# Kernel optimization log

Measured on AMD Instinct MI355X. Metric: run time of the kernel, lower is better.

Reference implementation:

```python
import jax, jax.numpy as jnp
import numpy as np

K = 3            # mc_sampling_steps
ALPHA = 0.5      # importance-weight decay
LAMBDA_COV = 0.5
EPS = 1e-8


def setup_inputs() -> dict:
    key = jax.random.key(0)
    k1, k2, k3, k4 = jax.random.split(key, 4)
    B, S, Et, Es, Ht, Hs = 8, 4096, 128, 16, 2048, 1024
    tg = jax.random.uniform(k1, (B, S, Et)) + 1e-3
    tg = tg / tg.sum(-1, keepdims=True)          # teacher gate probs
    sg = jax.random.uniform(k2, (B, S, Es)) + 1e-3
    sg = sg / sg.sum(-1, keepdims=True)          # student gate probs
    th = jax.random.normal(k3, (B, S, Ht))
    sh = jax.random.normal(k4, (B, S, Hs))
    am = jnp.ones((B, S), dtype=jnp.int32)       # all tokens valid
    return {"teacher_gates": tg, "student_gates": sg,
            "teacher_hidden_states": th, "student_hidden_states": sh,
            "attention_mask": am}


def _method_a(teacher_gates, student_gates, attention_mask):
    B, S, Et = teacher_gates.shape
    Es = student_gates.shape[-1]
    N = B * S
    tp = teacher_gates.reshape(N, Et)                 # flat teacher probs [N, Et]
    sp = student_gates.reshape(N, Es)                 # flat student probs [N, Es]
    log_sp = jnp.log(sp)
    vm = attention_mask.reshape(N).astype(tp.dtype)   # valid-token mask [N]
    carry_f = Et // Es                                # expert_dist[::carry] stride
    rows = jnp.arange(N)

    def step(carry, _):
        probs, key = carry
        key, sub = jax.random.split(key)
        idx = jax.random.categorical(sub, jnp.log(probs), axis=-1)        # multinomial [N]
        w = jnp.take_along_axis(probs, idx[:, None], axis=1)[:, 0]        # importance wt
        new = probs.at[rows, idx].multiply(ALPHA)                         # damp sampled expert
        new = new / new.sum(-1, keepdims=True)
        return (new, key), (idx, w)

    (_, _), (idxs, ws) = jax.lax.scan(step, (tp, jax.random.key(42)), None, length=K)
    ws = ws * vm[None, :]                             # [K, N]

    # KL(one_hot(idx)[::carry] || student) = -log sp[i, idx//carry] iff idx % carry == 0
    sidx = jnp.clip(idxs // carry_f, 0, Es - 1)
    hit = (idxs % carry_f) == 0
    kl = jnp.where(hit, -log_sp[rows[None, :], sidx], 0.0)                # [K, N]
    total_weight = ws.sum()
    feat_loss = (kl * ws).sum() / jnp.maximum(total_weight, EPS)

    # expert coverage counts (only teacher experts with index < Es contribute)
    in_range = (idxs < Es).astype(tp.dtype)
    t_counts = jnp.zeros(Et, tp.dtype).at[idxs.reshape(-1)].add((ws * in_range).reshape(-1))
    sval = sp[rows[None, :], jnp.clip(idxs, 0, Es - 1)] * in_range * vm[None, :]
    s_counts = jnp.zeros(Et, tp.dtype).at[idxs.reshape(-1)].add(sval.reshape(-1))

    ta = t_counts / t_counts.sum()
    sa = s_counts / s_counts.sum()
    ta = (ta + EPS); ta = ta / ta.sum()
    sa = (sa + EPS); sa = sa / sa.sum()
    coverage_kl = jnp.sum(ta * (jnp.log(ta) - jnp.log(sa))) / Et          # batchmean over Et
    return feat_loss, coverage_kl, feat_loss + LAMBDA_COV * coverage_kl


def reference(teacher_gates, student_gates, teacher_hidden_states, student_hidden_states, attention_mask):
    # enable_method_a=True, enable_method_b=False -> expert_total_loss == method_a_total_loss
    _, _, total = _method_a(teacher_gates, student_gates, attention_mask)
    return total
```

## Files before the change

### kernel.cpp

```cpp
#include <hip/hip_runtime.h>
#include <stdint.h>

#define ET 128
#define ES 16
#define ACC_STRIDE 258
#define ACC_USED 34
#define MAX_REPL 64

__host__ __device__ inline uint32_t rotl32(uint32_t x, int r) {
#ifdef __HIP_DEVICE_COMPILE__
  return __builtin_amdgcn_alignbit(x, x, (uint32_t)(32 - r));
#else
  return (x << r) | (x >> (32 - r));
#endif
}

__host__ __device__ inline void tf2x32(uint32_t k0, uint32_t k1,
                                       uint32_t& x0, uint32_t& x1) {
  uint32_t ks2 = k0 ^ k1 ^ 0x1BD11BDAu;
  x0 += k0; x1 += k1;
#define TF_ROT(r) { x0 += x1; x1 = rotl32(x1, r); x1 ^= x0; }
  TF_ROT(13) TF_ROT(15) TF_ROT(26) TF_ROT(6)
  x0 += k1;  x1 += ks2 + 1u;
  TF_ROT(17) TF_ROT(29) TF_ROT(16) TF_ROT(24)
  x0 += ks2; x1 += k0 + 2u;
  TF_ROT(13) TF_ROT(15) TF_ROT(26) TF_ROT(6)
  x0 += k0;  x1 += k1 + 3u;
  TF_ROT(17) TF_ROT(29) TF_ROT(16) TF_ROT(24)
  x0 += k1;  x1 += ks2 + 4u;
  TF_ROT(13) TF_ROT(15) TF_ROT(26) TF_ROT(6)
  x0 += ks2; x1 += k0 + 5u;
#undef TF_ROT
}

__device__ inline float unif01(uint32_t s0, uint32_t s1, uint32_t j) {
  uint32_t x0 = 0u, x1 = j;
  tf2x32(s0, s1, x0, x1);
  uint32_t bits = x0 ^ x1;
  float f = __uint_as_float((bits >> 9) | 0x3F800000u) - 1.0f;
  const float TINY = 1.17549435e-38f;
  return fmaxf(TINY, f + TINY);
}

__launch_bounds__(256)
__global__ void sample_kernel(const float* __restrict__ tg,
                              const float* __restrict__ sg,
                              const int* __restrict__ am,
                              double* __restrict__ acc,
                              unsigned int* __restrict__ done,
                              float* __restrict__ out,
                              int repl,
                              uint32_t s00, uint32_t s01,
                              uint32_t s10, uint32_t s11,
                              uint32_t s20, uint32_t s21,
                              int N, int total_waves) {
  __shared__ float lds_t[ES], lds_s[ES];
  __shared__ float lds_w[4], lds_kl[4];
  __shared__ int lds_last;
  __shared__ double tot[ACC_USED];
  if (threadIdx.x < ES) { lds_t[threadIdx.x] = 0.f; lds_s[threadIdx.x] = 0.f; }
  __syncthreads();

  const int wslot = threadIdx.x >> 6;
  const int wid = blockIdx.x * 4 + wslot;
  const int lane = threadIdx.x & 63;
  const int gl = lane & 15;
  const int gbase = lane & 0x30;
  const int stride = total_waves * 4;

  float sum_w = 0.f, sum_kl = 0.f;

#define LOADT(BASE, P, SGV, VM)                                              \
  {                                                                          \
    int nr_ = (BASE) + (lane >> 4);                                          \
    int ok_ = (nr_ < N);                                                     \
    int n_ = ok_ ? nr_ : (N - 1);                                            \
    const float4* r4_ = (const float4*)(tg + (size_t)n_ * ET + gl * 8);      \
    float4 aa_ = r4_[0], bb_ = r4_[1];                                       \
    P[0] = aa_.x; P[1] = aa_.y; P[2] = aa_.z; P[3] = aa_.w;                  \
    P[4] = bb_.x; P[5] = bb_.y; P[6] = bb_.z; P[7] = bb_.w;                  \
    SGV = sg[(size_t)n_ * ES + gl];                                          \
    VM = ok_ ? (float)am[n_] : 0.f;                                          \
  }

#define STEP(KA, KB, LAST)                                                   \
  {                                                                          \
    float e[8];                                                              \
    _Pragma("unroll")                                                        \
    for (int q = 0; q < 8; ++q)                                              \
      e[q] = -__logf(unif01(KA, KB, jb + (uint32_t)q)) * inv[q];             \
    unsigned long long key = ~0ull, ko;                                      \
    _Pragma("unroll")                                                        \
    for (int q = 0; q < 8; ++q) {                                            \
      ko = ((unsigned long long)__float_as_uint(e[q]) << 32)                 \
           | (uint32_t)(ebase + q);                                          \
      if (ko < key) key = ko;                                                \
    }                                                                        \
    ko = __shfl_xor(key, 1); if (ko < key) key = ko;                         \
    ko = __shfl_xor(key, 2); if (ko < key) key = ko;                         \
    ko = __shfl_xor(key, 4); if (ko < key) key = ko;                         \
    ko = __shfl_xor(key, 8); if (ko < key) key = ko;                         \
    const int bi = (int)(key & 0xFFu);                                       \
    const int wl = bi >> 3, wslt = bi & 7;                                   \
    float pw = p[0];                                                         \
    _Pragma("unroll")                                                        \
    for (int q = 1; q < 8; ++q) pw = (wslt == q) ? p[q] : pw;                \
    float w_abs = __shfl(pw, gbase | wl);                                    \
    float sgkl = __shfl(sgv, gbase | wl);                                    \
    float sgcv = __shfl(sgv, gbase | (bi & 15));                             \
    float wsv = w_abs * __frcp_rn(t) * vm;                                   \
    const bool lead = (gl == 0);                                             \
    sum_w += lead ? wsv : 0.f;                                               \
    float klt = ((bi & 7) == 0) ? (-__logf(sgkl)) * wsv : 0.f;               \
    sum_kl += lead ? klt : 0.f;                                              \
    if (lead && bi < ES) {                                                   \
      atomicAdd(&lds_t[bi], wsv);                                            \
      atomicAdd(&lds_s[bi], sgcv * vm);                                      \
    }                                                                        \
    if (!(LAST)) {                                                           \
      const bool mt = (gl == wl);                                            \
      _Pragma("unroll")                                                      \
      for (int q = 0; q < 8; ++q) {                                          \
        bool hit = mt && (wslt == q);                                        \
        p[q] = hit ? p[q] * 0.5f : p[q];                                     \
        inv[q] = hit ? inv[q] * 2.0f : inv[q];                               \
      }                                                                      \
      t -= 0.5f * w_abs;                                                     \
    }                                                                        \
  }

  float p[8], sgv = 0.f, vm = 0.f;
  const int base0 = wid * 4;
  if (base0 < N) LOADT(base0, p, sgv, vm);

  for (int base = base0; base < N; base += stride) {
    const int nxt = base + stride;
    float pn[8] = {0, 0, 0, 0, 0, 0, 0, 0};
    float sgn = 0.f, vmn = 0.f;
    if (nxt < N) LOADT(nxt, pn, sgn, vmn);

    {
      int nr = base + (lane >> 4);
      int n_ = (nr < N) ? nr : (N - 1);
      const uint32_t jb = (uint32_t)n_ * ET + (uint32_t)(gl * 8);
      const int ebase = gl * 8;
      float inv[8];
#pragma unroll
      for (int q = 0; q < 8; ++q) inv[q] = __frcp_rn(p[q]);
      float t = 1.0f;
      STEP(s00, s01, 0)
      STEP(s10, s11, 0)
      STEP(s20, s21, 1)
    }

#pragma unroll
    for (int q = 0; q < 8; ++q) p[q] = pn[q];
    sgv = sgn; vm = vmn;
  }
#undef STEP
#undef LOADT

#pragma unroll
  for (int off = 32; off; off >>= 1) {
    sum_w += __shfl_xor(sum_w, off);
    sum_kl += __shfl_xor(sum_kl, off);
  }
  if (lane == 0) { lds_w[wslot] = sum_w; lds_kl[wslot] = sum_kl; }
  __syncthreads();

  double* slot = acc + (size_t)(blockIdx.x % repl) * ACC_STRIDE;
  if (threadIdx.x == 0) {
    atomicAdd(&slot[0], (double)(lds_w[0] + lds_w[1] + lds_w[2] + lds_w[3]));
    atomicAdd(&slot[1], (double)(lds_kl[0] + lds_kl[1] + lds_kl[2] + lds_kl[3]));
  }
  if (threadIdx.x < ES) {
    atomicAdd(&slot[2 + threadIdx.x], (double)lds_t[threadIdx.x]);
    atomicAdd(&slot[2 + ES + threadIdx.x], (double)lds_s[threadIdx.x]);
  }

  if (threadIdx.x == 0) {
    __threadfence();
    unsigned prev = atomicAdd(done, 1u);
    lds_last = (prev == (unsigned)(gridDim.x - 1)) ? 1 : 0;
  }
  __syncthreads();
  if (!lds_last) return;

  const int tid = threadIdx.x;
  if (tid < ACC_USED) tot[tid] = 0.0;
  __syncthreads();
  for (int idx = tid; idx < repl * ACC_USED; idx += 256) {
    int r = idx / ACC_USED, f = idx - r * ACC_USED;
    double v = __hip_atomic_load(&acc[(size_t)r * ACC_STRIDE + f],
                                 __ATOMIC_RELAXED, __HIP_MEMORY_SCOPE_AGENT);
    atomicAdd(&tot[f], v);
  }
  __syncthreads();

  const double EPSD = 1e-8;
  double tv = (tid < ES) ? tot[2 + tid] : 0.0;
  double sv = (tid < ES) ? tot[2 + ES + tid] : 0.0;
  double tsum = tv, ssum = sv;
#pragma unroll
  for (int off = 8; off; off >>= 1) {
    tsum += __shfl_xor(tsum, off);
    ssum += __shfl_xor(ssum, off);
  }
  double ta = tv / tsum + EPSD;
  double sa = sv / ssum + EPSD;
  double ta2 = (tid < ES) ? ta : 0.0;
  double sa2 = (tid < ES) ? sa : 0.0;
#pragma unroll
  for (int off = 8; off; off >>= 1) {
    ta2 += __shfl_xor(ta2, off);
    sa2 += __shfl_xor(sa2, off);
  }
  ta2 += (double)(ET - ES) * EPSD;
  sa2 += (double)(ET - ES) * EPSD;
  double tn = ta / ta2, sn = sa / sa2;
  double ci = (tid < ES) ? tn * (log(tn) - log(sn)) : 0.0;
#pragma unroll
  for (int off = 8; off; off >>= 1) ci += __shfl_xor(ci, off);

  if (tid == 0) {
    double ta0 = EPSD / ta2, sa0 = EPSD / sa2;
    double cov = ci + (double)(ET - ES) * ta0 * (log(ta0) - log(sa0));
    cov /= (double)ET;
    double feat = tot[1] / fmax(tot[0], EPSD);
    out[0] = (float)(feat + 0.5 * cov);
  }
}

extern "C" void kernel_launch(void* const* d_in, const int* in_sizes, int n_in,
                              void* d_out, int out_size, void* d_ws, size_t ws_size,
                              hipStream_t stream) {
  const float* tg = (const float*)d_in[0];
  const float* sg = (const float*)d_in[1];
  const int*   am = (const int*)d_in[4];
  const int N = in_sizes[4];

  uint32_t key0 = 0u, key1 = 42u;
  uint32_t subs[3][2];
  for (int k = 0; k < 3; ++k) {
    uint32_t a0 = 0u, a1 = 0u; tf2x32(key0, key1, a0, a1);
    uint32_t b0 = 0u, b1 = 1u; tf2x32(key0, key1, b0, b1);
    subs[k][0] = b0; subs[k][1] = b1;
    key0 = a0; key1 = a1;
  }

  int repl = (int)((ws_size - 256) / (ACC_STRIDE * sizeof(double)));
  if (repl > MAX_REPL) repl = MAX_REPL;
  if (repl < 1) repl = 1;

  double* acc = (double*)d_ws;
  unsigned int* done = (unsigned int*)((char*)d_ws + (size_t)repl * ACC_STRIDE * sizeof(double));
  hipMemsetAsync(d_ws, 0, (size_t)repl * ACC_STRIDE * sizeof(double) + 64, stream);

  int blocks = (N + 31) / 32;
  if (blocks > 2048) blocks = 2048;
  if (blocks < 1) blocks = 1;
  const int total_waves = blocks * 4;

  sample_kernel<<<blocks, 256, 0, stream>>>(
      tg, sg, am, acc, done, (float*)d_out, repl,
      subs[0][0], subs[0][1], subs[1][0], subs[1][1], subs[2][0], subs[2][1],
      N, total_waves);
}
```

Measured before the change: 52.21 us.

## Use DPP min-reduction, 32-bit keys, log2 sampling, and drop software prefetch

Switches the per-row argmin to 32-bit packed keys reduced with DPP row operations instead of 64-bit shuffles. It replaces -log with log2 times a folded -ln2/p factor, uses the approximate rcp, and drops the TINY clamp on the uniform. It also removes the register double-buffered prefetch, fixes the replica count at 16, and shrinks the grid so each block covers fewer rows. The truncated key mantissa and the missing clamp can change tie-breaking and edge cases relative to the reference.

```diff
diff --git a/kernel.cpp b/kernel.cpp
--- a/kernel.cpp
+++ b/kernel.cpp
@@ -5,7 +5,7 @@
 #define ES 16
 #define ACC_STRIDE 258
 #define ACC_USED 34
-#define MAX_REPL 64
+#define REPL 16
 
 __host__ __device__ inline uint32_t rotl32(uint32_t x, int r) {
 #ifdef __HIP_DEVICE_COMPILE__
@@ -33,13 +33,19 @@
 #undef TF_ROT
 }
 
-__device__ inline float unif01(uint32_t s0, uint32_t s1, uint32_t j) {
+__device__ inline float unif01m(uint32_t s0, uint32_t s1, uint32_t j) {
   uint32_t x0 = 0u, x1 = j;
   tf2x32(s0, s1, x0, x1);
   uint32_t bits = x0 ^ x1;
-  float f = __uint_as_float((bits >> 9) | 0x3F800000u) - 1.0f;
-  const float TINY = 1.17549435e-38f;
-  return fmaxf(TINY, f + TINY);
+  return __uint_as_float((bits >> 9) | 0x3F800000u) - 1.0f;
+}
+
+__device__ inline float fastrcp(float x) { return __builtin_amdgcn_rcpf(x); }
+
+template <int CTRL>
+__device__ inline uint32_t dpp32(uint32_t v) {
+  return (uint32_t)__builtin_amdgcn_update_dpp((int)v, (int)v, CTRL, 0xF, 0xF,
+                                               false);
 }
 
 __launch_bounds__(256)
@@ -49,7 +55,6 @@
                               double* __restrict__ acc,
                               unsigned int* __restrict__ done,
                               float* __restrict__ out,
-                              int repl,
                               uint32_t s00, uint32_t s01,
                               uint32_t s10, uint32_t s11,
                               uint32_t s20, uint32_t s21,
@@ -67,40 +72,30 @@
   const int gl = lane & 15;
   const int gbase = lane & 0x30;
   const int stride = total_waves * 4;
+  const float NLN2 = -0.69314718055994530942f;
 
   float sum_w = 0.f, sum_kl = 0.f;
-
-#define LOADT(BASE, P, SGV, VM)                                              \
-  {                                                                          \
-    int nr_ = (BASE) + (lane >> 4);                                          \
-    int ok_ = (nr_ < N);                                                     \
-    int n_ = ok_ ? nr_ : (N - 1);                                            \
-    const float4* r4_ = (const float4*)(tg + (size_t)n_ * ET + gl * 8);      \
-    float4 aa_ = r4_[0], bb_ = r4_[1];                                       \
-    P[0] = aa_.x; P[1] = aa_.y; P[2] = aa_.z; P[3] = aa_.w;                  \
-    P[4] = bb_.x; P[5] = bb_.y; P[6] = bb_.z; P[7] = bb_.w;                  \
-    SGV = sg[(size_t)n_ * ES + gl];                                          \
-    VM = ok_ ? (float)am[n_] : 0.f;                                          \
-  }
 
 #define STEP(KA, KB, LAST)                                                   \
   {                                                                          \
     float e[8];                                                              \
     _Pragma("unroll")                                                        \
     for (int q = 0; q < 8; ++q)                                              \
-      e[q] = -__logf(unif01(KA, KB, jb + (uint32_t)q)) * inv[q];             \
-    unsigned long long key = ~0ull, ko;                                      \
+      e[q] = __log2f(unif01m(KA, KB, jb + (uint32_t)q)) * invn[q];           \
+    uint32_t key = 0xFFFFFFFFu;                                              \
     _Pragma("unroll")                                                        \
     for (int q = 0; q < 8; ++q) {                                            \
-      ko = ((unsigned long long)__float_as_uint(e[q]) << 32)                 \
-           | (uint32_t)(ebase + q);                                          \
-      if (ko < key) key = ko;                                                \
-    }                                                                        \
-    ko = __shfl_xor(key, 1); if (ko < key) key = ko;                         \
-    ko = __shfl_xor(key, 2); if (ko < key) key = ko;                         \
-    ko = __shfl_xor(key, 4); if (ko < key) key = ko;                         \
-    ko = __shfl_xor(key, 8); if (ko < key) key = ko;                         \
-    const int bi = (int)(key & 0xFFu);                                       \
+      uint32_t kq = (__float_as_uint(e[q]) & 0xFFFFFF80u)                    \
+                    | (uint32_t)(ebase + q);                                 \
+      key = (kq < key) ? kq : key;                                           \
+    }                                                                        \
+    { uint32_t o;                                                            \
+      o = dpp32<0x128>(key); key = (o < key) ? o : key;       \
+      o = dpp32<0x124>(key); key = (o < key) ? o : key;       \
+      o = dpp32<0x122>(key); key = (o < key) ? o : key;       \
+      o = dpp32<0x121>(key); key = (o < key) ? o : key;       \
+    }                                                                        \
+    const int bi = (int)(key & 0x7Fu);                                       \
     const int wl = bi >> 3, wslt = bi & 7;                                   \
     float pw = p[0];                                                         \
     _Pragma("unroll")                                                        \
@@ -108,10 +103,10 @@
     float w_abs = __shfl(pw, gbase | wl);                                    \
     float sgkl = __shfl(sgv, gbase | wl);                                    \
     float sgcv = __shfl(sgv, gbase | (bi & 15));                             \
-    float wsv = w_abs * __frcp_rn(t) * vm;                                   \
+    float wsv = w_abs * fastrcp(t) * vm;                                     \
     const bool lead = (gl == 0);                                             \
     sum_w += lead ? wsv : 0.f;                                               \
-    float klt = ((bi & 7) == 0) ? (-__logf(sgkl)) * wsv : 0.f;               \
+    float klt = (wslt == 0) ? (-__logf(sgkl)) * wsv : 0.f;                   \
     sum_kl += lead ? klt : 0.f;                                              \
     if (lead && bi < ES) {                                                   \
       atomicAdd(&lds_t[bi], wsv);                                            \
@@ -123,42 +118,35 @@
       for (int q = 0; q < 8; ++q) {                                          \
         bool hit = mt && (wslt == q);                                        \
         p[q] = hit ? p[q] * 0.5f : p[q];                                     \
-        inv[q] = hit ? inv[q] * 2.0f : inv[q];                               \
+        invn[q] = hit ? invn[q] * 2.0f : invn[q];                            \
       }                                                                      \
       t -= 0.5f * w_abs;                                                     \
     }                                                                        \
   }
 
-  float p[8], sgv = 0.f, vm = 0.f;
-  const int base0 = wid * 4;
-  if (base0 < N) LOADT(base0, p, sgv, vm);
-
-  for (int base = base0; base < N; base += stride) {
-    const int nxt = base + stride;
-    float pn[8] = {0, 0, 0, 0, 0, 0, 0, 0};
-    float sgn = 0.f, vmn = 0.f;
-    if (nxt < N) LOADT(nxt, pn, sgn, vmn);
-
-    {
-      int nr = base + (lane >> 4);
-      int n_ = (nr < N) ? nr : (N - 1);
-      const uint32_t jb = (uint32_t)n_ * ET + (uint32_t)(gl * 8);
-      const int ebase = gl * 8;
-      float inv[8];
-#pragma unroll
-      for (int q = 0; q < 8; ++q) inv[q] = __frcp_rn(p[q]);
-      float t = 1.0f;
-      STEP(s00, s01, 0)
-      STEP(s10, s11, 0)
-      STEP(s20, s21, 1)
-    }
-
-#pragma unroll
-    for (int q = 0; q < 8; ++q) p[q] = pn[q];
-    sgv = sgn; vm = vmn;
+  for (int base = wid * 4; base < N; base += stride) {
+    const int nr = base + (lane >> 4);
+    const int ok = (nr < N);
+    const int n = ok ? nr : (N - 1);
+
+    const float4* r4 = (const float4*)(tg + (size_t)n * ET + gl * 8);
+    float4 aa = r4[0], bb = r4[1];
+    float p[8] = {aa.x, aa.y, aa.z, aa.w, bb.x, bb.y, bb.z, bb.w};
+    float sgv = sg[(size_t)n * ES + gl];
+    float vm = ok ? (float)am[n] : 0.f;
+
+    float invn[8];
+#pragma unroll
+    for (int q = 0; q < 8; ++q) invn[q] = NLN2 * fastrcp(p[q]);
+
+    float t = 1.0f;
+    const uint32_t jb = (uint32_t)n * ET + (uint32_t)(gl * 8);
+    const int ebase = gl * 8;
+    STEP(s00, s01, 0)
+    STEP(s10, s11, 0)
+    STEP(s20, s21, 1)
   }
 #undef STEP
-#undef LOADT
 
 #pragma unroll
   for (int off = 32; off; off >>= 1) {
@@ -168,7 +156,7 @@
   if (lane == 0) { lds_w[wslot] = sum_w; lds_kl[wslot] = sum_kl; }
   __syncthreads();
 
-  double* slot = acc + (size_t)(blockIdx.x % repl) * ACC_STRIDE;
+  double* slot = acc + (size_t)(blockIdx.x % REPL) * ACC_STRIDE;
   if (threadIdx.x == 0) {
     atomicAdd(&slot[0], (double)(lds_w[0] + lds_w[1] + lds_w[2] + lds_w[3]));
     atomicAdd(&slot[1], (double)(lds_kl[0] + lds_kl[1] + lds_kl[2] + lds_kl[3]));
@@ -187,13 +175,12 @@
   if (!lds_last) return;
 
   const int tid = threadIdx.x;
-  if (tid < ACC_USED) tot[tid] = 0.0;
-  __syncthreads();
-  for (int idx = tid; idx < repl * ACC_USED; idx += 256) {
-    int r = idx / ACC_USED, f = idx - r * ACC_USED;
-    double v = __hip_atomic_load(&acc[(size_t)r * ACC_STRIDE + f],
-                                 __ATOMIC_RELAXED, __HIP_MEMORY_SCOPE_AGENT);
-    atomicAdd(&tot[f], v);
+  if (tid < ACC_USED) {
+    double s = 0.0;
+    for (int r = 0; r < REPL; ++r)
+      s += __hip_atomic_load(&acc[(size_t)r * ACC_STRIDE + tid],
+                             __ATOMIC_RELAXED, __HIP_MEMORY_SCOPE_AGENT);
+    tot[tid] = s;
   }
   __syncthreads();
 
@@ -248,21 +235,18 @@
     key0 = a0; key1 = a1;
   }
 
-  int repl = (int)((ws_size - 256) / (ACC_STRIDE * sizeof(double)));
-  if (repl > MAX_REPL) repl = MAX_REPL;
-  if (repl < 1) repl = 1;
-
   double* acc = (double*)d_ws;
-  unsigned int* done = (unsigned int*)((char*)d_ws + (size_t)repl * ACC_STRIDE * sizeof(double));
-  hipMemsetAsync(d_ws, 0, (size_t)repl * ACC_STRIDE * sizeof(double) + 64, stream);
-
-  int blocks = (N + 31) / 32;
+  unsigned int* done = (unsigned int*)(acc + (size_t)REPL * ACC_STRIDE);
+  hipMemsetAsync(d_ws, 0, (size_t)REPL * ACC_STRIDE * sizeof(double) + 64,
+                 stream);
+
+  int blocks = (N + 15) / 16;
   if (blocks > 2048) blocks = 2048;
   if (blocks < 1) blocks = 1;
   const int total_waves = blocks * 4;
 
   sample_kernel<<<blocks, 256, 0, stream>>>(
-      tg, sg, am, acc, done, (float*)d_out, repl,
+      tg, sg, am, acc, done, (float*)d_out,
       subs[0][0], subs[0][1], subs[1][0], subs[1][1], subs[2][0], subs[2][1],
       N, total_waves);
 }
```

New measurement: 50.25 us. 3.8% less time.
